# Kernel tuning notes

Hardware: AMD Instinct MI355X
Metric: run time of the kernel (lower is better)

The kernel has to match this reference:

```python
import jax, jax.numpy as jnp
import numpy as np

WS = 8      # window_size
C = 60      # channels
EXP = 2     # exp_ratio
DEPTH = 2   # 1 + shared_depth
B, H, W = 4, 256, 256
BN_EPS = 1e-5


def setup_inputs() -> dict:
    key = jax.random.key(0)
    ks = jax.random.split(key, 15)
    def rn(k, shape, s=0.1):
        return jax.random.normal(k, shape, jnp.float32) * s
    Ce = C * EXP
    return {
        "x": jax.random.normal(ks[0], (B, C, H, W), jnp.float32),
        "lfe_w0": rn(ks[1], (DEPTH, Ce, C)),
        "lfe_b0": rn(ks[2], (DEPTH, Ce)),
        "lfe_w1": rn(ks[3], (DEPTH, C, Ce)),
        "lfe_b1": rn(ks[4], (DEPTH, C)),
        "pi_w": rn(ks[5], (DEPTH, C, C)),
        "pi_b": rn(ks[6], (DEPTH, C)),
        "bn_g": 1.0 + rn(ks[7], (DEPTH, C)),
        "bn_b": rn(ks[8], (DEPTH, C)),
        "bn_m": rn(ks[9], (DEPTH, C)),
        "bn_v": jax.random.uniform(ks[10], (DEPTH, C), jnp.float32, 0.5, 1.5),
        "mask_w": rn(ks[11], (DEPTH, C, C)),
        "mask_b": rn(ks[12], (DEPTH, C)),
        "po_w": rn(ks[13], (DEPTH, C, C)),
        "po_b": rn(ks[14], (DEPTH, C)),
    }


def _conv1x1(x, w, b):
    # x: (b,c,h,w), w: (o,c)
    return jnp.einsum('oc,bchw->bohw', w, x) + b[None, :, None, None]


def _shift(x):
    # Faithful to ShiftConv2d1: depthwise 3x3 with one-hot kernels, zero pad=1.
    c = x.shape[1]; g = c // 5
    xp = jnp.pad(x, ((0, 0), (0, 0), (1, 1), (1, 1)))
    return jnp.concatenate([
        xp[:, 0 * g:1 * g, 1:-1, 2:],    # kernel (1,2): in[i, j+1]
        xp[:, 1 * g:2 * g, 1:-1, :-2],   # kernel (1,0): in[i, j-1]
        xp[:, 2 * g:3 * g, 2:, 1:-1],    # kernel (2,1): in[i+1, j]
        xp[:, 3 * g:4 * g, :-2, 1:-1],   # kernel (0,1): in[i-1, j]
        x[:, 4 * g:],                    # kernel (1,1): identity
    ], axis=1)


def _lfe(x, w0, b0, w1, b1):
    y = _conv1x1(_shift(x), w0, b0)
    y = jax.nn.gelu(y, approximate=False)  # torch nn.GELU() is exact erf
    return _conv1x1(_shift(y), w1, b1)


def _wsa(x, pi_w, pi_b, g, bt, m, v, mw, mb, pw, pb):
    b, c, h, w = x.shape; ws = WS
    # project_inp: 1x1 conv + BatchNorm2d (eval-mode stats)
    t = _conv1x1(x, pi_w, pi_b)
    scale = (g / jnp.sqrt(v + BN_EPS))
    t = (t - m[None, :, None, None]) * scale[None, :, None, None] + bt[None, :, None, None]
    # seq_refl_win_pad (forward): pad right/bottom by ws, then copy the
    # preceding ws-wide band into the padded region (rows first, then cols).
    xp = jnp.pad(t, ((0, 0), (0, 0), (0, ws), (0, ws)))
    xp = xp.at[:, :, -ws:, :].set(xp[:, :, -2 * ws:-ws, :])
    xp = xp.at[:, :, :, -ws:].set(xp[:, :, :, -2 * ws:-ws])
    nh, nw = h // ws, w // ws
    R = (jnp.arange(nh) * ws)[:, None] + jnp.arange(2 * ws)   # (nh, 2ws)
    Cc = (jnp.arange(nw) * ws)[:, None] + jnp.arange(2 * ws)  # (nw, 2ws)
    win = xp[:, :, R[:, None, :, None], Cc[None, :, None, :]]  # (b,c,nh,nw,2ws,2ws)
    # torch .unfold(3,..).unfold(2,..) yields window axes ordered (W-dir, H-dir)
    win = jnp.swapaxes(win, -1, -2)
    # 1x1 conv stride 2 == subsample every other pixel then 1x1 conv
    sub = win[..., ::2, ::2]  # (b,c,nh,nw,ws,ws)
    q = jnp.einsum('oc,bcijpq->bijpqo', mw, sub) + mb          # (b,nh,nw,ws,ws,c)
    q = q.reshape(b * nh * nw, ws * ws, c)
    vv = t.reshape(b, c, nh, ws, nw, ws).transpose(0, 2, 4, 3, 5, 1)
    vv = vv.reshape(b * nh * nw, ws * ws, c)
    atn = jax.nn.softmax(jnp.einsum('npc,nqc->npq', q, q), axis=-1)
    y = jnp.einsum('npq,nqc->npc', atn, vv)
    y = y.reshape(b, nh, nw, ws, ws, c).transpose(0, 5, 1, 3, 2, 4).reshape(b, c, h, w)
    return _conv1x1(y, pw, pb)


def reference(x, lfe_w0, lfe_b0, lfe_w1, lfe_b1, pi_w, pi_b, bn_g, bn_b, bn_m, bn_v, mask_w, mask_b, po_w, po_b):
    for i in range(DEPTH):
        x = _lfe(x, lfe_w0[i], lfe_b0[i], lfe_w1[i], lfe_b1[i]) + x
        x = _wsa(x, pi_w[i], pi_b[i], bn_g[i], bn_b[i], bn_m[i], bn_v[i],
                 mask_w[i], mask_b[i], po_w[i], po_b[i]) + x
    return x
```

## Files before the change

### kernel.cpp

```cpp
#include <hip/hip_runtime.h>
#include <math.h>

#define Hh 256
#define Ww 256
#define HW 65536
#define Bn 4
#define Cdim 60
#define Ce 120
#define NPIX (Bn*HW)

typedef const float* fp;

__device__ __forceinline__ float gelu_exact(float x){
  return 0.5f*x*(1.f + erff(x*0.70710678118654752f));
}

__device__ __forceinline__ void tile_decode(int blk, int& b, int& h, int& tw){
  b = blk >> 10; int rem = blk & 1023; h = rem >> 2; tw = (rem & 3) << 6;
}

__global__ __launch_bounds__(256) void k_lfe1(const float* __restrict__ X, float* __restrict__ Y1,
                                              fp w0, fp b0){
  __shared__ __align__(16) float A[60*64];
  __shared__ __align__(16) float Wt[60*132];
  int tid = threadIdx.x;
  int b, h, tw; tile_decode(blockIdx.x, b, h, tw);
  const float* Xb = X + (size_t)b*(Cdim*HW);
  for (int idx = tid; idx < 60*64; idx += 256){
    int k = idx >> 6, p = idx & 63;
    int grp = k / 12;
    int hh = h, ww = tw + p; bool ok = true;
    if (grp == 0){ ww += 1; ok = (ww < Ww); }
    else if (grp == 1){ ww -= 1; ok = (ww >= 0); }
    else if (grp == 2){ hh = h+1; ok = (hh < Hh); }
    else if (grp == 3){ hh = h-1; ok = (hh >= 0); }
    A[idx] = ok ? Xb[k*HW + hh*Ww + ww] : 0.f;
  }
  for (int idx = tid; idx < 120*60; idx += 256){
    int o = idx / 60, k = idx - o*60;
    Wt[k*132 + o] = w0[idx];
  }
  __syncthreads();
  if (tid < 240){
    int p0 = (tid & 15)*4;
    int o0 = (tid >> 4)*8;
    float acc[8][4];
    #pragma unroll
    for (int oi = 0; oi < 8; oi++){
      float bb = b0[o0+oi];
      #pragma unroll
      for (int pi = 0; pi < 4; pi++) acc[oi][pi] = bb;
    }
    #pragma unroll 4
    for (int k = 0; k < 60; k++){
      float4 a4 = *(const float4*)(&A[k*64 + p0]);
      float av[4] = {a4.x,a4.y,a4.z,a4.w};
      float4 wa = *(const float4*)(&Wt[k*132 + o0]);
      float4 wb = *(const float4*)(&Wt[k*132 + o0 + 4]);
      float wv[8] = {wa.x,wa.y,wa.z,wa.w, wb.x,wb.y,wb.z,wb.w};
      #pragma unroll
      for (int oi = 0; oi < 8; oi++){
        #pragma unroll
        for (int pi = 0; pi < 4; pi++)
          acc[oi][pi] += wv[oi]*av[pi];
      }
    }
    float* Yb = Y1 + (size_t)b*(Ce*HW) + h*Ww + tw + p0;
    #pragma unroll
    for (int oi = 0; oi < 8; oi++){
      float4 r;
      r.x = gelu_exact(acc[oi][0]); r.y = gelu_exact(acc[oi][1]);
      r.z = gelu_exact(acc[oi][2]); r.w = gelu_exact(acc[oi][3]);
      *(float4*)(Yb + (size_t)(o0+oi)*HW) = r;
    }
  }
}

__global__ __launch_bounds__(256) void k_lfe2(const float* __restrict__ Y1,
                                              const float* __restrict__ R,
                                              float* __restrict__ X,
                                              fp w1, fp b1){
  __shared__ __align__(16) float A[60*64];
  __shared__ __align__(16) float Wt[120*68];
  int tid = threadIdx.x;
  int b, h, tw; tile_decode(blockIdx.x, b, h, tw);
  const float* Yb = Y1 + (size_t)b*(Ce*HW);
  for (int idx = tid; idx < 60*120; idx += 256){
    int c = idx / 120, e = idx - c*120;
    Wt[e*68 + c] = w1[idx];
  }
  int p0 = (tid & 15)*4;
  int o0 = (tid >> 4)*4;
  float acc[4][4];
  #pragma unroll
  for (int oi = 0; oi < 4; oi++)
    #pragma unroll
    for (int pi = 0; pi < 4; pi++) acc[oi][pi] = 0.f;
  #pragma unroll 1
  for (int half = 0; half < 2; half++){
    __syncthreads();
    for (int idx = tid; idx < 60*64; idx += 256){
      int k = idx >> 6, p = idx & 63;
      int e = half*60 + k;
      int grp = e / 24;
      int hh = h, ww = tw + p; bool ok = true;
      if (grp == 0){ ww += 1; ok = (ww < Ww); }
      else if (grp == 1){ ww -= 1; ok = (ww >= 0); }
      else if (grp == 2){ hh = h+1; ok = (hh < Hh); }
      else if (grp == 3){ hh = h-1; ok = (hh >= 0); }
      A[idx] = ok ? Yb[e*HW + hh*Ww + ww] : 0.f;
    }
    __syncthreads();
    if (tid < 240){
      #pragma unroll 4
      for (int k = 0; k < 60; k++){
        float4 a4 = *(const float4*)(&A[k*64 + p0]);
        float av[4] = {a4.x,a4.y,a4.z,a4.w};
        float4 w4 = *(const float4*)(&Wt[(half*60 + k)*68 + o0]);
        float wv[4] = {w4.x,w4.y,w4.z,w4.w};
        #pragma unroll
        for (int oi = 0; oi < 4; oi++){
          #pragma unroll
          for (int pi = 0; pi < 4; pi++)
            acc[oi][pi] += wv[oi]*av[pi];
        }
      }
    }
  }
  if (tid < 240){
    const float* Rp = R + (size_t)b*(Cdim*HW) + h*Ww + tw + p0;
    float* Xp = X + (size_t)b*(Cdim*HW) + h*Ww + tw + p0;
    #pragma unroll
    for (int oi = 0; oi < 4; oi++){
      int o = o0 + oi;
      float bb = b1[o];
      float4 r4 = *(const float4*)(Rp + (size_t)o*HW);
      float4 out;
      out.x = acc[oi][0] + bb + r4.x;
      out.y = acc[oi][1] + bb + r4.y;
      out.z = acc[oi][2] + bb + r4.z;
      out.w = acc[oi][3] + bb + r4.w;
      *(float4*)(Xp + (size_t)o*HW) = out;
    }
  }
}

__global__ __launch_bounds__(256) void k_wsat(const float* __restrict__ X, float* __restrict__ T,
                                              fp piw, fp pib, fp g, fp bt, fp m, fp v){
  __shared__ __align__(16) float A[60*64];
  __shared__ __align__(16) float Wt[60*68];
  int tid = threadIdx.x;
  int b, h, tw; tile_decode(blockIdx.x, b, h, tw);
  const float* Xb = X + (size_t)b*(Cdim*HW) + h*Ww + tw;
  for (int idx = tid; idx < 60*64; idx += 256){
    int k = idx >> 6, p = idx & 63;
    A[idx] = Xb[k*HW + p];
  }
  for (int idx = tid; idx < 60*60; idx += 256){
    int o = idx / 60, k = idx - o*60;
    float scale = g[o] * rsqrtf(v[o] + 1e-5f);
    Wt[k*68 + o] = piw[idx] * scale;
  }
  __syncthreads();
  if (tid < 240){
    int p0 = (tid & 15)*4;
    int o0 = (tid >> 4)*4;
    float acc[4][4];
    #pragma unroll
    for (int oi = 0; oi < 4; oi++)
      #pragma unroll
      for (int pi = 0; pi < 4; pi++) acc[oi][pi] = 0.f;
    #pragma unroll 4
    for (int k = 0; k < 60; k++){
      float4 a4 = *(const float4*)(&A[k*64 + p0]);
      float av[4] = {a4.x,a4.y,a4.z,a4.w};
      float4 w4 = *(const float4*)(&Wt[k*68 + o0]);
      float wv[4] = {w4.x,w4.y,w4.z,w4.w};
      #pragma unroll
      for (int oi = 0; oi < 4; oi++){
        #pragma unroll
        for (int pi = 0; pi < 4; pi++)
          acc[oi][pi] += wv[oi]*av[pi];
      }
    }
    float* Tb = T + (size_t)b*(Cdim*HW) + h*Ww + tw + p0;
    #pragma unroll
    for (int oi = 0; oi < 4; oi++){
      int o = o0 + oi;
      float scale = g[o] * rsqrtf(v[o] + 1e-5f);
      float cns   = (pib[o] - m[o])*scale + bt[o];
      float4 out;
      out.x = acc[oi][0] + cns;
      out.y = acc[oi][1] + cns;
      out.z = acc[oi][2] + cns;
      out.w = acc[oi][3] + cns;
      *(float4*)(Tb + (size_t)o*HW) = out;
    }
  }
}

__global__ __launch_bounds__(256) void k_attn(const float* __restrict__ T, float* __restrict__ Y,
                                              fp mw, fp mb){
  __shared__ __align__(16) float R1[64*68];
  __shared__ __align__(16) float R2[64*68];
  __shared__ __align__(16) float R3[60*64];
  int tid = threadIdx.x;
  int blk = blockIdx.x;
  int b = blk >> 10; int ij = blk & 1023; int wi = ij >> 5; int wj = ij & 31;
  const float* Tb = T + (size_t)b*(Cdim*HW);

  for (int idx = tid; idx < Cdim*64; idx += 256){
    int k = idx >> 6, p = idx & 63;
    int u = p >> 3, vq = p & 7;
    int r  = wi*8 + 2*vq; if (r > 255) r -= 8;
    int cc = wj*8 + 2*u;  if (cc > 255) cc -= 8;
    R1[k*68 + p] = Tb[k*HW + r*Ww + cc];
  }
  for (int idx = tid; idx < Cdim*Cdim; idx += 256){
    int c = idx / Cdim, k = idx - c*Cdim;
    R2[c*61 + k] = mw[idx];
  }
  __syncthreads();

  if (tid < 240){
    int p0 = (tid & 15)*4, c0 = (tid >> 4)*4;
    float4 mb4 = *(const float4*)(mb + c0);
    float bias[4] = {mb4.x, mb4.y, mb4.z, mb4.w};
    float acc[4][4];
    #pragma unroll
    for (int ci = 0; ci < 4; ci++)
      #pragma unroll
      for (int pi = 0; pi < 4; pi++) acc[ci][pi] = bias[ci];
    #pragma unroll 4
    for (int k = 0; k < Cdim; k++){
      float4 a4 = *(const float4*)(&R1[k*68 + p0]);
      float av[4] = {a4.x, a4.y, a4.z, a4.w};
      #pragma unroll
      for (int ci = 0; ci < 4; ci++){
        float wv = R2[(c0+ci)*61 + k];
        #pragma unroll
        for (int pi = 0; pi < 4; pi++)
          acc[ci][pi] += wv*av[pi];
      }
    }
    #pragma unroll
    for (int ci = 0; ci < 4; ci++)
      *(float4*)(&R3[(c0+ci)*64 + p0]) = make_float4(acc[ci][0], acc[ci][1], acc[ci][2], acc[ci][3]);
  }
  __syncthreads();

  {
    int p = tid & 63; int cg = tid >> 6;
    int pr = p >> 3, pc = p & 7;
    const float* base = Tb + (wi*8+pr)*Ww + (wj*8+pc);
    #pragma unroll
    for (int t2 = 0; t2 < 15; t2++)
      R1[p*68 + cg*15 + t2] = base[(cg*15+t2)*HW];
  }
  if (tid < 64){
    R1[tid*68 + 60] = 0.f; R1[tid*68 + 61] = 0.f;
    R1[tid*68 + 62] = 0.f; R1[tid*68 + 63] = 0.f;
  }
  {
    int p0 = (tid & 15)*4, q0 = (tid >> 4)*4;
    float acc[4][4];
    #pragma unroll
    for (int qi = 0; qi < 4; qi++)
      #pragma unroll
      for (int pi = 0; pi < 4; pi++) acc[qi][pi] = 0.f;
    #pragma unroll 4
    for (int c = 0; c < Cdim; c++){
      float4 A4 = *(const float4*)(&R3[c*64 + p0]);
      float4 B4 = *(const float4*)(&R3[c*64 + q0]);
      float Af[4] = {A4.x, A4.y, A4.z, A4.w};
      float Bf[4] = {B4.x, B4.y, B4.z, B4.w};
      #pragma unroll
      for (int qi = 0; qi < 4; qi++)
        #pragma unroll
        for (int pi = 0; pi < 4; pi++)
          acc[qi][pi] += Bf[qi]*Af[pi];
    }
    __syncthreads();
    #pragma unroll
    for (int qi = 0; qi < 4; qi++)
      *(float4*)(&R2[(q0+qi)*68 + p0]) = make_float4(acc[qi][0], acc[qi][1], acc[qi][2], acc[qi][3]);
  }
  __syncthreads();

  {
    int p = tid & 63, gq = tid >> 6;
    float* Sc = R3;
    float mx = -1e30f;
    #pragma unroll
    for (int i = 0; i < 16; i++) mx = fmaxf(mx, R2[(gq*16+i)*68 + p]);
    Sc[gq*64 + p] = mx;
    __syncthreads();
    float m0 = fmaxf(fmaxf(Sc[p], Sc[64+p]), fmaxf(Sc[128+p], Sc[192+p]));
    float sum = 0.f;
    #pragma unroll
    for (int i = 0; i < 16; i++){
      int q = gq*16 + i;
      float e = __expf(R2[q*68 + p] - m0);
      R2[q*68 + p] = e; sum += e;
    }
    Sc[256 + gq*64 + p] = sum;
    __syncthreads();
    float tot = (Sc[256+p] + Sc[320+p]) + (Sc[384+p] + Sc[448+p]);
    float inv = 1.f/tot;
    #pragma unroll
    for (int i = 0; i < 16; i++) R2[(gq*16+i)*68 + p] *= inv;
  }
  __syncthreads();

  {
    int p0 = (tid & 15)*4, c0 = (tid >> 4)*4;
    float acc[4][4];
    #pragma unroll
    for (int ci = 0; ci < 4; ci++)
      #pragma unroll
      for (int pi = 0; pi < 4; pi++) acc[ci][pi] = 0.f;
    #pragma unroll 4
    for (int q = 0; q < 64; q++){
      float4 S4 = *(const float4*)(&R2[q*68 + p0]);
      float4 V4 = *(const float4*)(&R1[q*68 + c0]);
      float Sf[4] = {S4.x, S4.y, S4.z, S4.w};
      float Vf[4] = {V4.x, V4.y, V4.z, V4.w};
      #pragma unroll
      for (int ci = 0; ci < 4; ci++)
        #pragma unroll
        for (int pi = 0; pi < 4; pi++)
          acc[ci][pi] += Sf[pi]*Vf[ci];
    }
    float* Yb = Y + (size_t)b*(Cdim*HW);
    #pragma unroll
    for (int ci = 0; ci < 4; ci++){
      int c = c0 + ci;
      if (c < Cdim){
        #pragma unroll
        for (int pi = 0; pi < 4; pi++){
          int p = p0 + pi;
          Yb[c*HW + (wi*8 + (p>>3))*Ww + wj*8 + (p&7)] = acc[ci][pi];
        }
      }
    }
  }
}

__global__ __launch_bounds__(256) void k_wsaout(const float* __restrict__ Y, float* __restrict__ X,
                                                fp pw, fp pb){
  __shared__ __align__(16) float A[60*64];
  __shared__ __align__(16) float Wt[60*68];
  int tid = threadIdx.x;
  int b, h, tw; tile_decode(blockIdx.x, b, h, tw);
  const float* Yb = Y + (size_t)b*(Cdim*HW) + h*Ww + tw;
  for (int idx = tid; idx < 60*64; idx += 256){
    int k = idx >> 6, p = idx & 63;
    A[idx] = Yb[k*HW + p];
  }
  for (int idx = tid; idx < 60*60; idx += 256){
    int o = idx / 60, k = idx - o*60;
    Wt[k*68 + o] = pw[idx];
  }
  __syncthreads();
  if (tid < 240){
    int p0 = (tid & 15)*4;
    int o0 = (tid >> 4)*4;
    float acc[4][4];
    #pragma unroll
    for (int oi = 0; oi < 4; oi++)
      #pragma unroll
      for (int pi = 0; pi < 4; pi++) acc[oi][pi] = 0.f;
    #pragma unroll 4
    for (int k = 0; k < 60; k++){
      float4 a4 = *(const float4*)(&A[k*64 + p0]);
      float av[4] = {a4.x,a4.y,a4.z,a4.w};
      float4 w4 = *(const float4*)(&Wt[k*68 + o0]);
      float wv[4] = {w4.x,w4.y,w4.z,w4.w};
      #pragma unroll
      for (int oi = 0; oi < 4; oi++){
        #pragma unroll
        for (int pi = 0; pi < 4; pi++)
          acc[oi][pi] += wv[oi]*av[pi];
      }
    }
    float* Xp = X + (size_t)b*(Cdim*HW) + h*Ww + tw + p0;
    #pragma unroll
    for (int oi = 0; oi < 4; oi++){
      int o = o0 + oi;
      float bb = pb[o];
      float4 r4 = *(const float4*)(Xp + (size_t)o*HW);
      float4 out;
      out.x = acc[oi][0] + bb + r4.x;
      out.y = acc[oi][1] + bb + r4.y;
      out.z = acc[oi][2] + bb + r4.z;
      out.w = acc[oi][3] + bb + r4.w;
      *(float4*)(Xp + (size_t)o*HW) = out;
    }
  }
}

extern "C" void kernel_launch(void* const* d_in, const int* in_sizes, int n_in,
                              void* d_out, int out_size, void* d_ws, size_t ws_size,
                              hipStream_t stream){
  fp x      = (fp)d_in[0];
  fp lfe_w0 = (fp)d_in[1];
  fp lfe_b0 = (fp)d_in[2];
  fp lfe_w1 = (fp)d_in[3];
  fp lfe_b1 = (fp)d_in[4];
  fp pi_w   = (fp)d_in[5];
  fp pi_b   = (fp)d_in[6];
  fp bn_g   = (fp)d_in[7];
  fp bn_b   = (fp)d_in[8];
  fp bn_m   = (fp)d_in[9];
  fp bn_v   = (fp)d_in[10];
  fp mask_w = (fp)d_in[11];
  fp mask_b = (fp)d_in[12];
  fp po_w   = (fp)d_in[13];
  fp po_b   = (fp)d_in[14];

  const size_t XSZ = (size_t)Bn*Cdim*HW;
  float* X  = (float*)d_out;
  float* Y1 = (float*)d_ws;
  float* T  = Y1;
  float* Yw = Y1 + XSZ;

  const int NT = NPIX/64;

  for (int d = 0; d < 2; d++){
    fp src = (d == 0) ? x : X;
    k_lfe1  <<<NT, 256, 0, stream>>>(src, Y1, lfe_w0 + d*Ce*Cdim, lfe_b0 + d*Ce);
    k_lfe2  <<<NT, 256, 0, stream>>>(Y1, src, X, lfe_w1 + d*Ce*Cdim, lfe_b1 + d*Cdim);
    k_wsat  <<<NT, 256, 0, stream>>>(X, T, pi_w + d*Cdim*Cdim, pi_b + d*Cdim,
                                     bn_g + d*Cdim, bn_b + d*Cdim, bn_m + d*Cdim, bn_v + d*Cdim);
    k_attn  <<<Bn*32*32, 256, 0, stream>>>(T, Yw, mask_w + d*Cdim*Cdim, mask_b + d*Cdim);
    k_wsaout<<<NT, 256, 0, stream>>>(Yw, X, po_w + d*Cdim*Cdim, po_b + d*Cdim);
  }
}
```

Measured before the change: 1.060 ms.

## Fuse output projection and residual add into window attention kernel

The 1x1 output projection, its bias and the residual add are moved into the attention kernel. They run on the per-window attention result held in shared memory, so the intermediate attention output tensor is no longer written to and re-read from global memory. The separate output kernel launch goes away. In exchange the attention kernel gains a second shared-memory matmul and extra barriers, and writes to X in 8x8 window order rather than row tiles.

```diff
diff --git a/kernel.cpp b/kernel.cpp
--- a/kernel.cpp
+++ b/kernel.cpp
@@ -199,8 +199,8 @@
   }
 }
 
-__global__ __launch_bounds__(256) void k_attn(const float* __restrict__ T, float* __restrict__ Y,
-                                              fp mw, fp mb){
+__global__ __launch_bounds__(256) void k_attn(const float* __restrict__ T, float* __restrict__ X,
+                                              fp mw, fp mb, fp pw, fp pb){
   __shared__ __align__(16) float R1[64*68];
   __shared__ __align__(16) float R2[64*68];
   __shared__ __align__(16) float R3[60*64];
@@ -331,69 +331,51 @@
         for (int pi = 0; pi < 4; pi++)
           acc[ci][pi] += Sf[pi]*Vf[ci];
     }
-    float* Yb = Y + (size_t)b*(Cdim*HW);
-    #pragma unroll
-    for (int ci = 0; ci < 4; ci++){
-      int c = c0 + ci;
-      if (c < Cdim){
-        #pragma unroll
-        for (int pi = 0; pi < 4; pi++){
-          int p = p0 + pi;
-          Yb[c*HW + (wi*8 + (p>>3))*Ww + wj*8 + (p&7)] = acc[ci][pi];
-        }
+    __syncthreads();
+    if (c0 < Cdim){
+      #pragma unroll
+      for (int ci = 0; ci < 4; ci++)
+        *(float4*)(&R2[(c0+ci)*68 + p0]) = make_float4(acc[ci][0], acc[ci][1], acc[ci][2], acc[ci][3]);
+    }
+  }
+  for (int idx = tid; idx < Cdim*Cdim; idx += 256){
+    int o = idx / Cdim, k = idx - o*Cdim;
+    R1[k*68 + o] = pw[idx];
+  }
+  __syncthreads();
+
+  if (tid < 240){
+    int p0 = (tid & 15)*4, o0 = (tid >> 4)*4;
+    float acc2[4][4];
+    #pragma unroll
+    for (int oi = 0; oi < 4; oi++)
+      #pragma unroll
+      for (int pi = 0; pi < 4; pi++) acc2[oi][pi] = 0.f;
+    #pragma unroll 4
+    for (int k = 0; k < Cdim; k++){
+      float4 y4 = *(const float4*)(&R2[k*68 + p0]);
+      float4 w4 = *(const float4*)(&R1[k*68 + o0]);
+      float yv[4] = {y4.x,y4.y,y4.z,y4.w};
+      float wv[4] = {w4.x,w4.y,w4.z,w4.w};
+      #pragma unroll
+      for (int oi = 0; oi < 4; oi++){
+        #pragma unroll
+        for (int pi = 0; pi < 4; pi++)
+          acc2[oi][pi] += wv[oi]*yv[pi];
       }
     }
-  }
-}
-
-__global__ __launch_bounds__(256) void k_wsaout(const float* __restrict__ Y, float* __restrict__ X,
-                                                fp pw, fp pb){
-  __shared__ __align__(16) float A[60*64];
-  __shared__ __align__(16) float Wt[60*68];
-  int tid = threadIdx.x;
-  int b, h, tw; tile_decode(blockIdx.x, b, h, tw);
-  const float* Yb = Y + (size_t)b*(Cdim*HW) + h*Ww + tw;
-  for (int idx = tid; idx < 60*64; idx += 256){
-    int k = idx >> 6, p = idx & 63;
-    A[idx] = Yb[k*HW + p];
-  }
-  for (int idx = tid; idx < 60*60; idx += 256){
-    int o = idx / 60, k = idx - o*60;
-    Wt[k*68 + o] = pw[idx];
-  }
-  __syncthreads();
-  if (tid < 240){
-    int p0 = (tid & 15)*4;
-    int o0 = (tid >> 4)*4;
-    float acc[4][4];
-    #pragma unroll
-    for (int oi = 0; oi < 4; oi++)
-      #pragma unroll
-      for (int pi = 0; pi < 4; pi++) acc[oi][pi] = 0.f;
-    #pragma unroll 4
-    for (int k = 0; k < 60; k++){
-      float4 a4 = *(const float4*)(&A[k*64 + p0]);
-      float av[4] = {a4.x,a4.y,a4.z,a4.w};
-      float4 w4 = *(const float4*)(&Wt[k*68 + o0]);
-      float wv[4] = {w4.x,w4.y,w4.z,w4.w};
-      #pragma unroll
-      for (int oi = 0; oi < 4; oi++){
-        #pragma unroll
-        for (int pi = 0; pi < 4; pi++)
-          acc[oi][pi] += wv[oi]*av[pi];
-      }
-    }
-    float* Xp = X + (size_t)b*(Cdim*HW) + h*Ww + tw + p0;
+    int prow = wi*8 + (p0 >> 3), pcol = wj*8 + (p0 & 7);
+    float* Xp = X + (size_t)b*(Cdim*HW) + prow*Ww + pcol;
     #pragma unroll
     for (int oi = 0; oi < 4; oi++){
       int o = o0 + oi;
       float bb = pb[o];
       float4 r4 = *(const float4*)(Xp + (size_t)o*HW);
       float4 out;
-      out.x = acc[oi][0] + bb + r4.x;
-      out.y = acc[oi][1] + bb + r4.y;
-      out.z = acc[oi][2] + bb + r4.z;
-      out.w = acc[oi][3] + bb + r4.w;
+      out.x = acc2[oi][0] + bb + r4.x;
+      out.y = acc2[oi][1] + bb + r4.y;
+      out.z = acc2[oi][2] + bb + r4.z;
+      out.w = acc2[oi][3] + bb + r4.w;
       *(float4*)(Xp + (size_t)o*HW) = out;
     }
   }
@@ -422,7 +404,6 @@
   float* X  = (float*)d_out;
   float* Y1 = (float*)d_ws;
   float* T  = Y1;
-  float* Yw = Y1 + XSZ;
 
   const int NT = NPIX/64;
 
@@ -432,7 +413,7 @@
     k_lfe2  <<<NT, 256, 0, stream>>>(Y1, src, X, lfe_w1 + d*Ce*Cdim, lfe_b1 + d*Cdim);
     k_wsat  <<<NT, 256, 0, stream>>>(X, T, pi_w + d*Cdim*Cdim, pi_b + d*Cdim,
                                      bn_g + d*Cdim, bn_b + d*Cdim, bn_m + d*Cdim, bn_v + d*Cdim);
-    k_attn  <<<Bn*32*32, 256, 0, stream>>>(T, Yw, mask_w + d*Cdim*Cdim, mask_b + d*Cdim);
-    k_wsaout<<<NT, 256, 0, stream>>>(Yw, X, po_w + d*Cdim*Cdim, po_b + d*Cdim);
-  }
-}
+    k_attn  <<<Bn*32*32, 256, 0, stream>>>(T, X, mask_w + d*Cdim*Cdim, mask_b + d*Cdim,
+                                           po_w + d*Cdim*Cdim, po_b + d*Cdim);
+  }
+}
```

Result: no change. 1.064 ms (+0.5%).
